# Kernel tuning notes

Hardware: AMD Instinct MI355X
Metric: run time of the kernel (lower is better)

## Reference

```python
import jax, jax.numpy as jnp
import numpy as np

DIM = 2048
NC = 12  # n_components (hard-coded in module)
EPS = 1e-5


def setup_inputs() -> dict:
    key = jax.random.key(0)
    ks = jax.random.split(key, 8)
    s = lambda fan_in: 1.0 / np.sqrt(fan_in)
    return {
        "x": jax.random.normal(ks[0], (8, 4096, DIM), dtype=jnp.float32),
        "Wp": jax.random.uniform(ks[1], (DIM, NC), jnp.float32, -s(DIM), s(DIM)),
        "bp": jax.random.uniform(ks[2], (NC,), jnp.float32, -s(DIM), s(DIM)),
        "Wv": jax.random.uniform(ks[3], (DIM, NC), jnp.float32, -s(DIM), s(DIM)),
        "bv": jax.random.uniform(ks[4], (NC,), jnp.float32, -s(DIM), s(DIM)),
        "Wi": jax.random.uniform(ks[5], (NC * NC, DIM), jnp.float32, -s(NC * NC), s(NC * NC)),
        "bi": jax.random.uniform(ks[6], (DIM,), jnp.float32, -s(NC * NC), s(NC * NC)),
        "gamma": jnp.ones((DIM,), jnp.float32),
        "beta": jnp.zeros((DIM,), jnp.float32),
    }


def reference(x, Wp, bp, Wv, bv, Wi, bi, gamma, beta):
    B, N, D = x.shape
    pos = x @ Wp + bp                      # [B,N,12]
    vel = x @ Wv + bv                      # [B,N,12]
    inter = jnp.einsum('bni,bnj->bnij', pos, vel).reshape(B, N, NC * NC)
    inter = inter @ Wi + bi                # [B,N,D]
    y = x + inter
    mu = jnp.mean(y, axis=-1, keepdims=True)
    var = jnp.mean(jnp.square(y - mu), axis=-1, keepdims=True)
    return (y - mu) * jax.lax.rsqrt(var + EPS) * gamma + beta
```

## Files before the change

### kernel.cpp

```cpp
#include <hip/hip_runtime.h>

#define D 2048
#define KPAD 160
#define PSTR 168
#define XSTR 2056
#define MTILE 16
#define THREADS 512

typedef __attribute__((ext_vector_type(8))) short bf16x8;
typedef __attribute__((ext_vector_type(4))) float f32x4;

__device__ inline unsigned short f2bf(float f) {
  unsigned int u = __float_as_uint(f);
  u += 0x7fffu + ((u >> 16) & 1u);
  return (unsigned short)(u >> 16);
}
__device__ inline float bf2f(unsigned short h) {
  return __uint_as_float(((unsigned int)h) << 16);
}

__global__ __launch_bounds__(256) void prep_wpv(const float* __restrict__ Wp,
                                                const float* __restrict__ Wv,
                                                unsigned short* __restrict__ Wpvt) {
  int idx = blockIdx.x * 256 + threadIdx.x;
  int n = idx >> 11, k = idx & 2047;
  float v = 0.f;
  if (n < 12) v = Wp[k * 12 + n];
  else if (n < 24) v = Wv[k * 12 + (n - 12)];
  Wpvt[idx] = f2bf(v);
}

__global__ __launch_bounds__(256) void prep_wi(const float* __restrict__ Wi,
                                               unsigned short* __restrict__ Wit) {
  int idx = blockIdx.x * 256 + threadIdx.x;
  int n = idx / KPAD, k = idx - n * KPAD;
  float v = (k < 144) ? Wi[k * 2048 + n] : 0.f;
  Wit[idx] = f2bf(v);
}

__global__ __launch_bounds__(THREADS, 4) void gil_fused(
    const float* __restrict__ x, const float* __restrict__ bp,
    const float* __restrict__ bv, const float* __restrict__ bi,
    const float* __restrict__ gamma, const float* __restrict__ beta,
    const unsigned short* __restrict__ Wpvt, const unsigned short* __restrict__ Wit,
    float* __restrict__ out) {
  __shared__ unsigned short xt[MTILE][XSTR];
  __shared__ unsigned short sP[MTILE][PSTR];
  __shared__ __align__(16) unsigned char ured[8192];
  float (*sred)[MTILE][32] = (float (*)[MTILE][32])ured;
  float (*spart)[MTILE][2] = (float (*)[MTILE][2])ured;
  float (*sstat)[2]        = (float (*)[2])(ured + 4096);

  const int t = threadIdx.x;
  const int rowbase = blockIdx.x * MTILE;

  {
    int r = t >> 5, u = t & 31;
    const float4* xr = (const float4*)(x + (size_t)(rowbase + r) * D);
#pragma unroll
    for (int j = 0; j < 16; ++j) {
      float4 v = xr[u + 32 * j];
      ushort4 p;
      p.x = f2bf(v.x); p.y = f2bf(v.y); p.z = f2bf(v.z); p.w = f2bf(v.w);
      *(ushort4*)&xt[r][4 * (u + 32 * j)] = p;
    }
  }
  __syncthreads();

  const int wave = t >> 6, lane = t & 63;
  const int lm = lane & 15, quad = lane >> 4;

  {
    int nt = wave & 1, ks = wave >> 1;
    f32x4 acc = {0.f, 0.f, 0.f, 0.f};
    const unsigned short* bptr = Wpvt + (nt * 16 + lm) * D;
#pragma unroll
    for (int kk = 0; kk < 16; ++kk) {
      int k0 = ks * 512 + kk * 32 + quad * 8;
      bf16x8 a = *(const bf16x8*)&xt[lm][k0];
      bf16x8 b = *(const bf16x8*)(bptr + k0);
      acc = __builtin_amdgcn_mfma_f32_16x16x32_bf16(a, b, acc, 0, 0, 0);
    }
#pragma unroll
    for (int rg = 0; rg < 4; ++rg)
      sred[ks][quad * 4 + rg][nt * 16 + lm] = acc[rg];
  }
  __syncthreads();

  {
    int m = t >> 5, n = t & 31;
    float pv = sred[0][m][n] + sred[1][m][n] + sred[2][m][n] + sred[3][m][n];
    if (n < 12) pv += bp[n];
    else if (n < 24) pv += bv[n - 12];
#pragma unroll
    for (int kk = 0; kk < 5; ++kk) {
      int k = n + 32 * kk;
      int i = k / 12, j = k - i * 12;
      float a = __shfl(pv, i, 32);
      float b = __shfl(pv, 12 + j, 32);
      sP[m][k] = f2bf((k < 144) ? a * b : 0.f);
    }
  }
  __syncthreads();

  f32x4 accv[16];
  {
    bf16x8 af[5];
#pragma unroll
    for (int kc = 0; kc < 5; ++kc)
      af[kc] = *(const bf16x8*)&sP[lm][kc * 32 + quad * 8];
#pragma unroll
    for (int nt = 0; nt < 16; ++nt) {
      int n = wave * 256 + nt * 16 + lm;
      const unsigned short* wb = Wit + n * KPAD;
      f32x4 acc = {0.f, 0.f, 0.f, 0.f};
#pragma unroll
      for (int kc = 0; kc < 5; ++kc) {
        bf16x8 b = *(const bf16x8*)(wb + kc * 32 + quad * 8);
        acc = __builtin_amdgcn_mfma_f32_16x16x32_bf16(af[kc], b, acc, 0, 0, 0);
      }
      accv[nt] = acc;
    }
  }

  float s[4] = {0.f, 0.f, 0.f, 0.f}, ss[4] = {0.f, 0.f, 0.f, 0.f};
#pragma unroll
  for (int nt = 0; nt < 16; ++nt) {
    int c = wave * 256 + nt * 16 + lm;
    float bic = bi[c];
#pragma unroll
    for (int rg = 0; rg < 4; ++rg) {
      int row = quad * 4 + rg;
      float y = accv[nt][rg] + bic + bf2f(xt[row][c]);
      accv[nt][rg] = y;
      s[rg] += y;
      ss[rg] += y * y;
    }
  }
#pragma unroll
  for (int off = 1; off < 16; off <<= 1) {
#pragma unroll
    for (int rg = 0; rg < 4; ++rg) {
      s[rg] += __shfl_xor(s[rg], off);
      ss[rg] += __shfl_xor(ss[rg], off);
    }
  }
  if (lm == 0) {
#pragma unroll
    for (int rg = 0; rg < 4; ++rg) {
      spart[wave][quad * 4 + rg][0] = s[rg];
      spart[wave][quad * 4 + rg][1] = ss[rg];
    }
  }
  __syncthreads();
  if (t < MTILE) {
    float su = 0.f, sq = 0.f;
#pragma unroll
    for (int w = 0; w < 8; ++w) { su += spart[w][t][0]; sq += spart[w][t][1]; }
    float mu = su * (1.f / D);
    float var = sq * (1.f / D) - mu * mu;
    sstat[t][0] = mu;
    sstat[t][1] = rsqrtf(var + 1e-5f);
  }
  __syncthreads();

  float mu[4], rs[4];
#pragma unroll
  for (int rg = 0; rg < 4; ++rg) {
    mu[rg] = sstat[quad * 4 + rg][0];
    rs[rg] = sstat[quad * 4 + rg][1];
  }
#pragma unroll
  for (int nt = 0; nt < 16; ++nt) {
    int c = wave * 256 + nt * 16 + lm;
    float g = gamma[c], be = beta[c];
#pragma unroll
    for (int rg = 0; rg < 4; ++rg) {
      int row = quad * 4 + rg;
      out[(size_t)(rowbase + row) * D + c] = (accv[nt][rg] - mu[rg]) * rs[rg] * g + be;
    }
  }
}

extern "C" void kernel_launch(void* const* d_in, const int* in_sizes, int n_in,
                              void* d_out, int out_size, void* d_ws, size_t ws_size,
                              hipStream_t stream) {
  const float* x     = (const float*)d_in[0];
  const float* Wp    = (const float*)d_in[1];
  const float* bp    = (const float*)d_in[2];
  const float* Wv    = (const float*)d_in[3];
  const float* bv    = (const float*)d_in[4];
  const float* Wi    = (const float*)d_in[5];
  const float* bi    = (const float*)d_in[6];
  const float* gamma = (const float*)d_in[7];
  const float* beta  = (const float*)d_in[8];
  float* out = (float*)d_out;

  unsigned short* Wpvt = (unsigned short*)d_ws;
  unsigned short* Wit  = Wpvt + 32 * 2048;

  prep_wpv<<<(32 * 2048) / 256, 256, 0, stream>>>(Wp, Wv, Wpvt);
  prep_wi<<<(2048 * KPAD) / 256, 256, 0, stream>>>(Wi, Wit);

  int rows = in_sizes[0] / D;
  gil_fused<<<rows / MTILE, THREADS, 0, stream>>>(x, bp, bv, bi, gamma, beta,
                                                  Wpvt, Wit, out);
}
```

Measured before the change: 556.0 us.

## Drop shared x tile, load x directly and transpose MFMA output for vector stores

Removes the 64KB shared bf16 copy of the x tile. The projection GEMM now reads fp32 x straight from global and converts it in registers, with each wave covering its own K slice. The interaction GEMM swaps its A/B operands so each lane holds 4 consecutive columns of one row. This enables float4 loads of x, bi, gamma and beta, float4 output stores, and a simpler row reduction. The residual now uses exact fp32 x instead of bf16. The trade-off is that x is re-read from global (likely an L2 hit) in exchange for much lower LDS use, which should raise occupancy.

```diff
diff --git a/kernel.cpp b/kernel.cpp
--- a/kernel.cpp
+++ b/kernel.cpp
@@ -3,7 +3,6 @@
 #define D 2048
 #define KPAD 160
 #define PSTR 168
-#define XSTR 2056
 #define MTILE 16
 #define THREADS 512
 
@@ -14,9 +13,6 @@
   unsigned int u = __float_as_uint(f);
   u += 0x7fffu + ((u >> 16) & 1u);
   return (unsigned short)(u >> 16);
-}
-__device__ inline float bf2f(unsigned short h) {
-  return __uint_as_float(((unsigned int)h) << 16);
 }
 
 __global__ __launch_bounds__(256) void prep_wpv(const float* __restrict__ Wp,
@@ -44,52 +40,50 @@
     const float* __restrict__ gamma, const float* __restrict__ beta,
     const unsigned short* __restrict__ Wpvt, const unsigned short* __restrict__ Wit,
     float* __restrict__ out) {
-  __shared__ unsigned short xt[MTILE][XSTR];
-  __shared__ unsigned short sP[MTILE][PSTR];
-  __shared__ __align__(16) unsigned char ured[8192];
-  float (*sred)[MTILE][32] = (float (*)[MTILE][32])ured;
-  float (*spart)[MTILE][2] = (float (*)[MTILE][2])ured;
-  float (*sstat)[2]        = (float (*)[2])(ured + 4096);
+  __shared__ float sred[8][MTILE][36];
+  __shared__ __align__(16) unsigned short sP[MTILE][PSTR];
+  __shared__ float spart[8][MTILE][2];
+  __shared__ float sstat[MTILE][2];
 
   const int t = threadIdx.x;
   const int rowbase = blockIdx.x * MTILE;
-
-  {
-    int r = t >> 5, u = t & 31;
-    const float4* xr = (const float4*)(x + (size_t)(rowbase + r) * D);
-#pragma unroll
-    for (int j = 0; j < 16; ++j) {
-      float4 v = xr[u + 32 * j];
-      ushort4 p;
-      p.x = f2bf(v.x); p.y = f2bf(v.y); p.z = f2bf(v.z); p.w = f2bf(v.w);
-      *(ushort4*)&xt[r][4 * (u + 32 * j)] = p;
-    }
-  }
-  __syncthreads();
-
   const int wave = t >> 6, lane = t & 63;
   const int lm = lane & 15, quad = lane >> 4;
 
   {
-    int nt = wave & 1, ks = wave >> 1;
-    f32x4 acc = {0.f, 0.f, 0.f, 0.f};
-    const unsigned short* bptr = Wpvt + (nt * 16 + lm) * D;
+    const float* xr = x + (size_t)(rowbase + lm) * D + wave * 256;
+    const unsigned short* b0 = Wpvt + (size_t)lm * D + wave * 256;
+    const unsigned short* b1 = Wpvt + (size_t)(16 + lm) * D + wave * 256;
+    f32x4 acc0 = {0.f, 0.f, 0.f, 0.f}, acc1 = {0.f, 0.f, 0.f, 0.f};
 #pragma unroll
-    for (int kk = 0; kk < 16; ++kk) {
-      int k0 = ks * 512 + kk * 32 + quad * 8;
-      bf16x8 a = *(const bf16x8*)&xt[lm][k0];
-      bf16x8 b = *(const bf16x8*)(bptr + k0);
-      acc = __builtin_amdgcn_mfma_f32_16x16x32_bf16(a, b, acc, 0, 0, 0);
+    for (int kk = 0; kk < 8; ++kk) {
+      int k0 = kk * 32 + quad * 8;
+      f32x4 v0 = *(const f32x4*)(xr + k0);
+      f32x4 v1 = *(const f32x4*)(xr + k0 + 4);
+      bf16x8 a;
+#pragma unroll
+      for (int e = 0; e < 4; ++e) {
+        a[e]     = (short)f2bf(v0[e]);
+        a[4 + e] = (short)f2bf(v1[e]);
+      }
+      bf16x8 w0 = *(const bf16x8*)(b0 + k0);
+      bf16x8 w1 = *(const bf16x8*)(b1 + k0);
+      acc0 = __builtin_amdgcn_mfma_f32_16x16x32_bf16(a, w0, acc0, 0, 0, 0);
+      acc1 = __builtin_amdgcn_mfma_f32_16x16x32_bf16(a, w1, acc1, 0, 0, 0);
     }
 #pragma unroll
-    for (int rg = 0; rg < 4; ++rg)
-      sred[ks][quad * 4 + rg][nt * 16 + lm] = acc[rg];
+    for (int rg = 0; rg < 4; ++rg) {
+      sred[wave][quad * 4 + rg][lm]      = acc0[rg];
+      sred[wave][quad * 4 + rg][16 + lm] = acc1[rg];
+    }
   }
   __syncthreads();
 
   {
     int m = t >> 5, n = t & 31;
-    float pv = sred[0][m][n] + sred[1][m][n] + sred[2][m][n] + sred[3][m][n];
+    float pv = 0.f;
+#pragma unroll
+    for (int w = 0; w < 8; ++w) pv += sred[w][m][n];
     if (n < 12) pv += bp[n];
     else if (n < 24) pv += bv[n - 12];
 #pragma unroll
@@ -105,52 +99,42 @@
 
   f32x4 accv[16];
   {
-    bf16x8 af[5];
+    bf16x8 bf[5];
 #pragma unroll
     for (int kc = 0; kc < 5; ++kc)
-      af[kc] = *(const bf16x8*)&sP[lm][kc * 32 + quad * 8];
+      bf[kc] = *(const bf16x8*)&sP[lm][kc * 32 + quad * 8];
 #pragma unroll
     for (int nt = 0; nt < 16; ++nt) {
-      int n = wave * 256 + nt * 16 + lm;
-      const unsigned short* wb = Wit + n * KPAD;
+      const unsigned short* wb = Wit + (size_t)(wave * 256 + nt * 16 + lm) * KPAD;
       f32x4 acc = {0.f, 0.f, 0.f, 0.f};
 #pragma unroll
       for (int kc = 0; kc < 5; ++kc) {
-        bf16x8 b = *(const bf16x8*)(wb + kc * 32 + quad * 8);
-        acc = __builtin_amdgcn_mfma_f32_16x16x32_bf16(af[kc], b, acc, 0, 0, 0);
+        bf16x8 wv = *(const bf16x8*)(wb + kc * 32 + quad * 8);
+        acc = __builtin_amdgcn_mfma_f32_16x16x32_bf16(wv, bf[kc], acc, 0, 0, 0);
       }
       accv[nt] = acc;
     }
   }
 
-  float s[4] = {0.f, 0.f, 0.f, 0.f}, ss[4] = {0.f, 0.f, 0.f, 0.f};
+  float s = 0.f, ss = 0.f;
+  {
+    const float* xrow = x + (size_t)(rowbase + lm) * D;
 #pragma unroll
-  for (int nt = 0; nt < 16; ++nt) {
-    int c = wave * 256 + nt * 16 + lm;
-    float bic = bi[c];
+    for (int nt = 0; nt < 16; ++nt) {
+      int d0 = wave * 256 + nt * 16 + quad * 4;
+      f32x4 bi4 = *(const f32x4*)(bi + d0);
+      f32x4 x4  = *(const f32x4*)(xrow + d0);
 #pragma unroll
-    for (int rg = 0; rg < 4; ++rg) {
-      int row = quad * 4 + rg;
-      float y = accv[nt][rg] + bic + bf2f(xt[row][c]);
-      accv[nt][rg] = y;
-      s[rg] += y;
-      ss[rg] += y * y;
+      for (int rg = 0; rg < 4; ++rg) {
+        float y = accv[nt][rg] + bi4[rg] + x4[rg];
+        accv[nt][rg] = y;
+        s += y;
+        ss += y * y;
+      }
     }
-  }
-#pragma unroll
-  for (int off = 1; off < 16; off <<= 1) {
-#pragma unroll
-    for (int rg = 0; rg < 4; ++rg) {
-      s[rg] += __shfl_xor(s[rg], off);
-      ss[rg] += __shfl_xor(ss[rg], off);
-    }
-  }
-  if (lm == 0) {
-#pragma unroll
-    for (int rg = 0; rg < 4; ++rg) {
-      spart[wave][quad * 4 + rg][0] = s[rg];
-      spart[wave][quad * 4 + rg][1] = ss[rg];
-    }
+    s += __shfl_xor(s, 16); ss += __shfl_xor(ss, 16);
+    s += __shfl_xor(s, 32); ss += __shfl_xor(ss, 32);
+    if (lane < 16) { spart[wave][lm][0] = s; spart[wave][lm][1] = ss; }
   }
   __syncthreads();
   if (t < MTILE) {
@@ -164,20 +148,19 @@
   }
   __syncthreads();
 
-  float mu[4], rs[4];
+  {
+    float mu = sstat[lm][0], rs = sstat[lm][1];
+    float* orow = out + (size_t)(rowbase + lm) * D;
 #pragma unroll
-  for (int rg = 0; rg < 4; ++rg) {
-    mu[rg] = sstat[quad * 4 + rg][0];
-    rs[rg] = sstat[quad * 4 + rg][1];
-  }
+    for (int nt = 0; nt < 16; ++nt) {
+      int d0 = wave * 256 + nt * 16 + quad * 4;
+      f32x4 g4  = *(const f32x4*)(gamma + d0);
+      f32x4 be4 = *(const f32x4*)(beta + d0);
+      f32x4 o;
 #pragma unroll
-  for (int nt = 0; nt < 16; ++nt) {
-    int c = wave * 256 + nt * 16 + lm;
-    float g = gamma[c], be = beta[c];
-#pragma unroll
-    for (int rg = 0; rg < 4; ++rg) {
-      int row = quad * 4 + rg;
-      out[(size_t)(rowbase + row) * D + c] = (accv[nt][rg] - mu[rg]) * rs[rg] * g + be;
+      for (int rg = 0; rg < 4; ++rg)
+        o[rg] = (accv[nt][rg] - mu) * rs * g4[rg] + be4[rg];
+      *(f32x4*)(orow + d0) = o;
     }
   }
 }
```

Result: slower. 641.0 us (+15.3%).
